# Optimization experiments

Measured on AMD Instinct MI355X. Metric: run time of the kernel, lower is better.

## Reference

```python
import jax, jax.numpy as jnp
import numpy as np

B, L, D = 2, 2048, 2048
NUM_HEADS, NUM_KV_HEADS, HEAD_DIM = 8, 4, 256
GROUPS = NUM_HEADS // NUM_KV_HEADS
ROPE_BASE, ROPE_SCALE, ROPE_PROP = 10000.0, 1.0, 1.0
WINDOW = 1024
SOFT_CAP = 50.0
K_MASK = -2.3819763e+38
EPS = 1e-6


def rms_norm(x, scale):
    # RMSNorm(head_dim, with_scale=True, scale_plus_one=False), fp32 internals
    xf = x.astype(jnp.float32)
    var = jnp.mean(jnp.square(xf), axis=-1, keepdims=True)
    return (xf * jax.lax.rsqrt(var + EPS) * scale).astype(x.dtype)


def apply_rope(x, positions):
    # x: [B, L, N, H]; Gemma-style half-split rotation over rope_proportion of H
    H = x.shape[-1]
    rope_dim = int(H * ROPE_PROP)
    half = rope_dim // 2
    freq = ROPE_BASE ** (2.0 * jnp.arange(half, dtype=jnp.float32) / rope_dim)
    t = positions.astype(jnp.float32)[:, :, None] / freq[None, None, :]  # [B,L,half]
    t = t / ROPE_SCALE
    sin = jnp.sin(t)[:, :, None, :]  # [B,L,1,half]
    cos = jnp.cos(t)[:, :, None, :]
    x1 = x[..., :half]
    x2 = x[..., half:rope_dim]
    rotated = jnp.concatenate([x1 * cos - x2 * sin, x2 * cos + x1 * sin], axis=-1)
    if rope_dim < H:
        rotated = jnp.concatenate([rotated, x[..., rope_dim:]], axis=-1)
    return rotated.astype(x.dtype)


def setup_inputs() -> dict:
    key = jax.random.key(0)
    ks = jax.random.split(key, 8)
    x = jax.random.normal(ks[0], (B, L, D), dtype=jnp.float32)
    positions = jnp.broadcast_to(jnp.arange(L, dtype=jnp.int32)[None, :], (B, L))
    attn_mask = jnp.broadcast_to(jnp.tril(jnp.ones((L, L), dtype=bool))[None], (B, L, L))
    s = 0.02
    wq = jax.random.normal(ks[1], (D, NUM_HEADS * HEAD_DIM), dtype=jnp.float32) * s
    wk = jax.random.normal(ks[2], (D, NUM_KV_HEADS * HEAD_DIM), dtype=jnp.float32) * s
    wv = jax.random.normal(ks[3], (D, NUM_KV_HEADS * HEAD_DIM), dtype=jnp.float32) * s
    wo = jax.random.normal(ks[4], (NUM_HEADS * HEAD_DIM, D), dtype=jnp.float32) * s
    q_scale = 1.0 + 0.02 * jax.random.normal(ks[5], (HEAD_DIM,), dtype=jnp.float32)
    k_scale = 1.0 + 0.02 * jax.random.normal(ks[6], (HEAD_DIM,), dtype=jnp.float32)
    return {"x": x, "positions": positions, "attn_mask": attn_mask,
            "wq": wq, "wk": wk, "wv": wv, "wo": wo,
            "q_scale": q_scale, "k_scale": k_scale}


def reference(x, positions, attn_mask, wq, wk, wv, wo, q_scale, k_scale):
    q = (x @ wq).reshape(B, L, NUM_HEADS, HEAD_DIM)
    k = (x @ wk).reshape(B, L, NUM_KV_HEADS, HEAD_DIM)
    v = (x @ wv).reshape(B, L, NUM_KV_HEADS, HEAD_DIM)
    q = rms_norm(q, q_scale)
    k = rms_norm(k, k_scale)
    q = apply_rope(q, positions)
    k = apply_rope(k, positions)
    # query_pre_attn_scalar == 1.0 in source (no-op)
    qg = q.reshape(B, L, NUM_KV_HEADS, GROUPS, HEAD_DIM)
    logits = jnp.einsum('blkgh,bskh->blkgs', qg, k).reshape(B, L, NUM_HEADS, L)
    logits = jnp.tanh(logits / SOFT_CAP) * SOFT_CAP
    # sliding-window mask (LOCAL_SLIDING, no cache -> cache_positions = positions)
    cp = positions[:, None, :]
    pp = positions[:, :, None]
    slide = (cp > pp - WINDOW) & (cp < pp + WINDOW)
    mask = attn_mask & slide  # [B, L, S]
    padded = jnp.where(mask[:, :, None, :], logits, K_MASK)
    probs = jax.nn.softmax(padded, axis=-1).astype(k.dtype)
    pg = probs.reshape(B, L, NUM_KV_HEADS, GROUPS, L)
    out = jnp.einsum('blkgs,bskh->blkgh', pg, v).reshape(B, L, NUM_HEADS * HEAD_DIM)
    return out @ wo
```

## Files before the change

kernel.cpp:

```cpp
#include <hip/hip_runtime.h>
#include <stdint.h>

typedef unsigned short u16;
typedef __bf16 bf16x8 __attribute__((ext_vector_type(8)));
typedef float f32x4 __attribute__((ext_vector_type(4)));

#define SEQ 2048
#define NH 8
#define NKVH 4
#define HD 256
#define WIN 1024
#define NBATCH 2

__device__ __forceinline__ u16 f2bf(float f) {
    union { float f; unsigned u; } v; v.f = f;
    unsigned r = v.u + 0x7FFFu + ((v.u >> 16) & 1u);
    return (u16)(r >> 16);
}
__device__ __forceinline__ float bf2f(u16 h) {
    union { unsigned u; float f; } v; v.u = ((unsigned)h) << 16;
    return v.f;
}
__device__ __forceinline__ bf16x8 ld8(const u16* p) {
    return *reinterpret_cast<const bf16x8*>(p);
}
__device__ __forceinline__ void split2(float f, u16& h, u16& l) {
    h = f2bf(f);
    l = f2bf(f - bf2f(h));
}
__device__ __forceinline__ void gld16(const u16* gp, u16* lp) {
    __builtin_amdgcn_global_load_lds(
        (__attribute__((address_space(1))) unsigned int*)gp,
        (__attribute__((address_space(3))) unsigned int*)lp, 16, 0, 0);
}
#define MFMA16(a, b, c) __builtin_amdgcn_mfma_f32_16x16x32_bf16((a), (b), (c), 0, 0, 0)

__global__ void k_cvt_x(const float* __restrict__ in, u16* __restrict__ hi,
                        u16* __restrict__ lo, int n) {
    int i = (blockIdx.x * blockDim.x + threadIdx.x) * 4;
    if (i >= n) return;
    float4 v = *reinterpret_cast<const float4*>(in + i);
    ushort4 oh, ol;
    split2(v.x, oh.x, ol.x); split2(v.y, oh.y, ol.y);
    split2(v.z, oh.z, ol.z); split2(v.w, oh.w, ol.w);
    *reinterpret_cast<ushort4*>(hi + i) = oh;
    *reinterpret_cast<ushort4*>(lo + i) = ol;
}

__global__ void k_wt(const float* __restrict__ src, u16* __restrict__ dh,
                     u16* __restrict__ dl, int ncols) {
    __shared__ float tile[64][65];
    int c0 = blockIdx.x * 64;
    int k0 = blockIdx.y * 64;
    int tx = threadIdx.x & 63, ty = threadIdx.x >> 6;
    #pragma unroll
    for (int r = 0; r < 16; ++r) {
        int k = k0 + ty * 16 + r;
        tile[ty * 16 + r][tx] = src[(size_t)k * ncols + c0 + tx];
    }
    __syncthreads();
    #pragma unroll
    for (int r = 0; r < 16; ++r) {
        int c = c0 + ty * 16 + r;
        float f = tile[tx][ty * 16 + r];
        u16 h, l; split2(f, h, l);
        dh[(size_t)c * 2048 + k0 + tx] = h;
        dl[(size_t)c * 2048 + k0 + tx] = l;
    }
}

__global__ __launch_bounds__(256, 4) void k_gemm(
        const u16* __restrict__ A0, const u16* __restrict__ B0,
        const u16* __restrict__ A1, const u16* __restrict__ B1,
        const u16* __restrict__ A2, const u16* __restrict__ B2,
        float* __restrict__ C, int M, int N, int K, int nseg, int vcol0) {
    __shared__ __align__(16) u16 sA[128 * 64];
    __shared__ __align__(16) u16 sB[128 * 64];
    const int tm = blockIdx.x * 128;
    const int tn = blockIdx.y * 128;
    const int tid = threadIdx.x;
    const int lane = tid & 63;
    const int wave = tid >> 6;
    const int wr = (wave >> 1) * 64;
    const int wc = (wave & 1) * 64;
    const int l16 = lane & 15;
    const int g = lane >> 4;
    const int srow = tid >> 3;
    const int schunk = tid & 7;
    const int nseg_eff = (tn >= vcol0) ? 1 : nseg;
    f32x4 acc[4][4] = {};

    for (int seg = 0; seg < nseg_eff; ++seg) {
        const u16* A = seg == 0 ? A0 : (seg == 1 ? A1 : A2);
        const u16* B = seg == 0 ? B0 : (seg == 1 ? B1 : B2);
        for (int k0 = 0; k0 < K; k0 += 64) {
            __syncthreads();
            #pragma unroll
            for (int i = 0; i < 4; ++i) {
                int row = i * 32 + srow;
                int cs = ((schunk ^ (row & 7)) << 3);
                gld16(A + (size_t)(tm + row) * K + k0 + cs, &sA[i * 2048 + tid * 8]);
                gld16(B + (size_t)(tn + row) * K + k0 + cs, &sB[i * 2048 + tid * 8]);
            }
            __syncthreads();
            #pragma unroll
            for (int kk = 0; kk < 2; ++kk) {
                const int j = kk * 4 + g;
                bf16x8 af[4], bfv[4];
                #pragma unroll
                for (int m = 0; m < 4; ++m) {
                    int r = wr + m * 16 + l16;
                    af[m] = ld8(&sA[r * 64 + ((j ^ (r & 7)) << 3)]);
                }
                #pragma unroll
                for (int n = 0; n < 4; ++n) {
                    int r = wc + n * 16 + l16;
                    bfv[n] = ld8(&sB[r * 64 + ((j ^ (r & 7)) << 3)]);
                }
                #pragma unroll
                for (int m = 0; m < 4; ++m)
                    #pragma unroll
                    for (int n = 0; n < 4; ++n)
                        acc[m][n] = MFMA16(af[m], bfv[n], acc[m][n]);
            }
        }
    }
    int rbase = tm + wr + g * 4;
    int cbase = tn + wc + l16;
    #pragma unroll
    for (int m = 0; m < 4; ++m)
        #pragma unroll
        for (int n = 0; n < 4; ++n)
            #pragma unroll
            for (int r = 0; r < 4; ++r)
                C[(size_t)(rbase + m * 16 + r) * N + cbase + n * 16] = acc[m][n][r];
}

__global__ __launch_bounds__(512, 2) void k_gemm256(
        const u16* __restrict__ A0, const u16* __restrict__ B0,
        const u16* __restrict__ A1, const u16* __restrict__ B1,
        const u16* __restrict__ A2, const u16* __restrict__ B2,
        float* __restrict__ C, int N, int K, int nseg, int vcol0) {
    __shared__ __align__(16) u16 sA[2][256 * 64];
    __shared__ __align__(16) u16 sB[2][256 * 64];
    const int tm = blockIdx.x * 256;
    const int tn = blockIdx.y * 256;
    const int tid = threadIdx.x;
    const int lane = tid & 63;
    const int wave = tid >> 6;
    const int wr = (wave >> 2) * 128;
    const int wc = (wave & 3) * 64;
    const int l16 = lane & 15;
    const int g = lane >> 4;
    const int nsteps = ((tn >= vcol0) ? 1 : nseg) * (K >> 6);
    const int spk = K >> 6;
    f32x4 acc[8][4] = {};

    {
        const u16* A = A0; const u16* B = B0;
        #pragma unroll
        for (int i = 0; i < 4; ++i) {
            int s = i * 512 + tid;
            int row = s >> 3, ch = s & 7;
            int cs = (ch ^ (row & 7)) << 3;
            gld16(A + (size_t)(tm + row) * K + cs, &sA[0][s * 8]);
            gld16(B + (size_t)(tn + row) * K + cs, &sB[0][s * 8]);
        }
    }
    asm volatile("s_waitcnt vmcnt(0)" ::: "memory");
    __builtin_amdgcn_s_barrier();

    int p = 0;
    for (int t = 0; t < nsteps; ++t) {
        if (t + 1 < nsteps) {
            int t1 = t + 1;
            int seg = t1 / spk;
            int k0 = (t1 - seg * spk) * 64;
            const u16* A = seg == 0 ? A0 : (seg == 1 ? A1 : A2);
            const u16* B = seg == 0 ? B0 : (seg == 1 ? B1 : B2);
            #pragma unroll
            for (int i = 0; i < 4; ++i) {
                int s = i * 512 + tid;
                int row = s >> 3, ch = s & 7;
                int cs = (ch ^ (row & 7)) << 3;
                gld16(A + (size_t)(tm + row) * K + k0 + cs, &sA[p ^ 1][s * 8]);
                gld16(B + (size_t)(tn + row) * K + k0 + cs, &sB[p ^ 1][s * 8]);
            }
        }
        __builtin_amdgcn_s_setprio(1);
        bf16x8 bfv[4][2];
        #pragma unroll
        for (int n = 0; n < 4; ++n)
            #pragma unroll
            for (int kk = 0; kk < 2; ++kk) {
                int r = wc + n * 16 + l16;
                int j = kk * 4 + g;
                bfv[n][kk] = ld8(&sB[p][r * 64 + ((j ^ (r & 7)) << 3)]);
            }
        #pragma unroll
        for (int m = 0; m < 8; ++m) {
            int r = wr + m * 16 + l16;
            bf16x8 af0 = ld8(&sA[p][r * 64 + (((0 * 4 + g) ^ (r & 7)) << 3)]);
            bf16x8 af1 = ld8(&sA[p][r * 64 + (((1 * 4 + g) ^ (r & 7)) << 3)]);
            #pragma unroll
            for (int n = 0; n < 4; ++n) {
                acc[m][n] = MFMA16(af0, bfv[n][0], acc[m][n]);
                acc[m][n] = MFMA16(af1, bfv[n][1], acc[m][n]);
            }
        }
        __builtin_amdgcn_s_setprio(0);
        asm volatile("s_waitcnt vmcnt(0) lgkmcnt(0)" ::: "memory");
        __builtin_amdgcn_sched_barrier(0);
        __builtin_amdgcn_s_barrier();
        p ^= 1;
    }

    int rbase = tm + wr + g * 4;
    int cbase = tn + wc + l16;
    #pragma unroll
    for (int m = 0; m < 8; ++m)
        #pragma unroll
        for (int n = 0; n < 4; ++n)
            #pragma unroll
            for (int r = 0; r < 4; ++r)
                C[(size_t)(rbase + m * 16 + r) * N + cbase + n * 16] = acc[m][n][r];
}

__global__ void k_normrope(const float* __restrict__ qkv, const int* __restrict__ pos,
                           const float* __restrict__ qscale, const float* __restrict__ kscale,
                           u16* __restrict__ Qh, u16* __restrict__ Ql,
                           u16* __restrict__ Kh, u16* __restrict__ Kl) {
    int wid = blockIdx.x * 4 + (threadIdx.x >> 6);
    int lane = threadIdx.x & 63;
    const int nq = NBATCH * SEQ * NH;
    const int ntot = NBATCH * SEQ * (NH + NKVH);
    if (wid >= ntot) return;
    const float* scale;
    const float* src;
    u16 *dh, *dl;
    int bt, isq;
    if (wid < nq) {
        int h = wid % NH; bt = wid / NH; isq = 1;
        scale = qscale;
        src = qkv + (size_t)bt * 4096 + h * 256;
        int b = bt >> 11, t = bt & 2047;
        size_t off = (((size_t)b * NH + h) * SEQ + t) * 256;
        dh = Qh + off; dl = Ql + off;
    } else {
        int w2 = wid - nq;
        int h = w2 % NKVH; bt = w2 / NKVH; isq = 0;
        scale = kscale;
        src = qkv + (size_t)bt * 4096 + 2048 + h * 256;
        int b = bt >> 11, t = bt & 2047;
        size_t off = (((size_t)b * NKVH + h) * SEQ + t) * 256;
        dh = Kh + off; dl = Kl + off;
    }
    const int t7 = bt & 7;
    float e[4];
    float ssq = 0.f;
    #pragma unroll
    for (int j = 0; j < 4; ++j) { e[j] = src[lane + 64 * j]; ssq += e[j] * e[j]; }
    #pragma unroll
    for (int off = 1; off < 64; off <<= 1) ssq += __shfl_xor(ssq, off);
    float inv = rsqrtf(ssq * (1.0f / 256.0f) + 1e-6f);
    #pragma unroll
    for (int j = 0; j < 4; ++j) e[j] = e[j] * inv * scale[lane + 64 * j];
    float p = (float)pos[bt];
    float fr0 = powf(10000.0f, (2.0f * lane) * (1.0f / 256.0f));
    float fr1 = powf(10000.0f, (2.0f * (lane + 64)) * (1.0f / 256.0f));
    float s0, c0, s1, c1;
    sincosf(p / fr0, &s0, &c0);
    sincosf(p / fr1, &s1, &c1);
    float rv[4];
    rv[0] = e[0] * c0 - e[2] * s0;
    rv[1] = e[1] * c1 - e[3] * s1;
    rv[2] = e[2] * c0 + e[0] * s0;
    rv[3] = e[3] * c1 + e[1] * s1;
    #pragma unroll
    for (int j = 0; j < 4; ++j) {
        int d = lane + 64 * j;
        int dd = isq ? d : ((((d >> 3) ^ t7) << 3) | (d & 7));
        u16 h, l; split2(rv[j], h, l);
        dh[dd] = h; dl[dd] = l;
    }
}

__global__ void k_vtrans(const float* __restrict__ qkv, u16* __restrict__ VT) {
    __shared__ float tile[64][65];
    int bh = blockIdx.z;
    int d0 = blockIdx.y * 64;
    int t0 = blockIdx.x * 64;
    int b = bh >> 2, h = bh & 3;
    int tx = threadIdx.x & 63, ty = threadIdx.x >> 6;
    #pragma unroll
    for (int r = 0; r < 16; ++r) {
        int t = t0 + ty * 16 + r;
        tile[ty * 16 + r][tx] = qkv[(size_t)(b * SEQ + t) * 4096 + 3072 + h * 256 + d0 + tx];
    }
    __syncthreads();
    #pragma unroll
    for (int r = 0; r < 16; ++r) {
        int d = d0 + ty * 16 + r;
        VT[((size_t)bh * 256 + d) * SEQ + t0 + tx] = f2bf(tile[tx][ty * 16 + r]);
    }
}

__global__ __launch_bounds__(256, 2) void k_attn(const u16* __restrict__ Qh, const u16* __restrict__ Ql,
                                                 const u16* __restrict__ Kh, const u16* __restrict__ Kl,
                                                 const u16* __restrict__ VT,
                                                 u16* __restrict__ Out) {
    __shared__ __align__(16) u16 sKh[32 * 256];
    __shared__ __align__(16) u16 sKl[32 * 256];
    __shared__ __align__(16) u16 sV[256 * 32];
    __shared__ __align__(16) u16 pls[4][16][40];

    const int id = blockIdx.x;
    const int xcd = id & 7;
    const int j = id >> 3;
    const int b  = xcd >> 2;
    const int hk = xcd & 3;
    const int hq = hk * 2 + (j & 1);
    const int qt = 31 - (j >> 1);
    const int tid = threadIdx.x;
    const int lane = tid & 63;
    const int wave = tid >> 6;
    const int q0b = qt * 64;
    const int q0 = q0b + wave * 16;
    const int l16 = lane & 15;
    const int g = lane >> 4;

    bf16x8 qfh[8], qfl[8];
    {
        size_t qoff = (((size_t)b * NH + hq) * SEQ + q0 + l16) * 256 + g * 8;
        #pragma unroll
        for (int kk = 0; kk < 8; ++kk) {
            qfh[kk] = ld8(Qh + qoff + kk * 32);
            qfl[kk] = ld8(Ql + qoff + kk * 32);
        }
    }

    float ssum[4] = {0.f, 0.f, 0.f, 0.f};
    f32x4 o[16] = {};

    const u16* kgh = Kh + (((size_t)b * NKVH + hk) * SEQ) * 256;
    const u16* kgl = Kl + (((size_t)b * NKVH + hk) * SEQ) * 256;
    const u16* vg  = VT + ((size_t)(b * NKVH + hk) * 256) * SEQ;

    int s_lo = q0b - (WIN - 1); if (s_lo < 0) s_lo = 0; s_lo &= ~31;
    const int s_hi = q0b + 63;
    const int ntiles = (s_hi - s_lo) / 32 + 1;

    for (int t = 0; t < ntiles; ++t) {
        const int s0 = s_lo + t * 32;
        __syncthreads();
        {
            const u16* srch = kgh + (size_t)s0 * 256 + tid * 8;
            const u16* srcl = kgl + (size_t)s0 * 256 + tid * 8;
            #pragma unroll
            for (int i = 0; i < 4; ++i) {
                gld16(srch + i * 2048, &sKh[i * 2048 + tid * 8]);
                gld16(srcl + i * 2048, &sKl[i * 2048 + tid * 8]);
            }
            const u16* srcv = vg + (size_t)(tid >> 2) * SEQ + s0 + (tid & 3) * 8;
            #pragma unroll
            for (int i = 0; i < 4; ++i)
                gld16(srcv + (size_t)i * 64 * SEQ, &sV[i * 2048 + tid * 8]);
        }
        __syncthreads();

        if (s0 <= q0 + 15 && s0 + 31 >= q0 - (WIN - 1)) {
            f32x4 c[2] = {};
            __builtin_amdgcn_s_setprio(1);
            #pragma unroll
            for (int kk = 0; kk < 8; ++kk) {
                #pragma unroll
                for (int cc = 0; cc < 2; ++cc) {
                    int row = cc * 16 + l16;
                    int slot = ((kk * 4 + g) ^ (row & 7)) << 3;
                    bf16x8 kh = ld8(&sKh[row * 256 + slot]);
                    bf16x8 kl = ld8(&sKl[row * 256 + slot]);
                    c[cc] = MFMA16(qfh[kk], kh, c[cc]);
                    c[cc] = MFMA16(qfl[kk], kh, c[cc]);
                    c[cc] = MFMA16(qfh[kk], kl, c[cc]);
                }
            }
            __builtin_amdgcn_s_setprio(0);

            const bool full = (s0 + 31 <= q0) && (s0 >= q0 + 15 - (WIN - 1));
            #pragma unroll
            for (int r = 0; r < 4; ++r) {
                int qp = q0 + g * 4 + r;
                int row = g * 4 + r;
                #pragma unroll
                for (int cc = 0; cc < 2; ++cc) {
                    float ev = __expf(c[cc][r] * 0.04f);
                    float v = 50.f - 100.f * __builtin_amdgcn_rcpf(ev + 1.f);
                    if (!full) {
                        int sp = s0 + cc * 16 + l16;
                        bool valid = (sp <= qp) && (sp > qp - WIN);
                        v = valid ? v : -1e30f;
                    }
                    float p = __expf(v - 20.f);
                    u16 pb = f2bf(p);
                    pls[wave][row][cc * 16 + l16] = pb;
                    ssum[r] += bf2f(pb);
                }
            }
            bf16x8 pa = ld8(&pls[wave][l16][g * 8]);
            __builtin_amdgcn_s_setprio(1);
            #pragma unroll
            for (int jb = 0; jb < 16; ++jb)
                o[jb] = MFMA16(pa, ld8(&sV[(jb * 16 + l16) * 32 + g * 8]), o[jb]);
            __builtin_amdgcn_s_setprio(0);
        }
    }

    #pragma unroll
    for (int off = 1; off < 16; off <<= 1)
        #pragma unroll
        for (int r = 0; r < 4; ++r) ssum[r] += __shfl_xor(ssum[r], off);
    #pragma unroll
    for (int r = 0; r < 4; ++r) {
        float inv = 1.0f / ssum[r];
        int trow = q0 + g * 4 + r;
        size_t base = ((size_t)(b * SEQ + trow) * NH + hq) * 256 + l16;
        #pragma unroll
        for (int jb = 0; jb < 16; ++jb)
            Out[base + jb * 16] = f2bf(o[jb][r] * inv);
    }
}

extern "C" void kernel_launch(void* const* d_in, const int* in_sizes, int n_in,
                              void* d_out, int out_size, void* d_ws, size_t ws_size,
                              hipStream_t stream) {
    (void)in_sizes; (void)n_in; (void)out_size; (void)ws_size;
    const float* x  = (const float*)d_in[0];
    const int* pos  = (const int*)d_in[1];
    const float* wq = (const float*)d_in[3];
    const float* wk = (const float*)d_in[4];
    const float* wv = (const float*)d_in[5];
    const float* wo = (const float*)d_in[6];
    const float* qs = (const float*)d_in[7];
    const float* ks = (const float*)d_in[8];

    const size_t MX = (size_t)4096 * 2048;
    const size_t MW = (size_t)2048 * 2048;

    u16* xh  = (u16*)d_ws;
    u16* xl  = xh + MX;
    u16* wth = xl + MX;
    u16* wtl = wth + MX;
    u16* woth = wtl + MX;
    u16* wotl = woth + MW;
    float* qkv = (float*)(wotl + MW);

    u16* qbh = xh;
    u16* qbl = qbh + MX;
    u16* kbh = qbl + MX;
    u16* kbl = kbh + MX / 2;
    u16* vt  = kbl + MX / 2;
    u16* ao  = (u16*)qkv;

    k_cvt_x<<<8192, 256, 0, stream>>>(x, xh, xl, 4096 * 2048);
    k_wt<<<dim3(32, 32), 256, 0, stream>>>(wq, wth, wtl, 2048);
    k_wt<<<dim3(16, 32), 256, 0, stream>>>(wk, wth + MW, wtl + MW, 1024);
    k_wt<<<dim3(16, 32), 256, 0, stream>>>(wv, wth + MW + MW / 2, wtl + MW + MW / 2, 1024);
    k_wt<<<dim3(32, 32), 256, 0, stream>>>(wo, woth, wotl, 2048);
    k_gemm256<<<dim3(16, 16), 512, 0, stream>>>(xh, wth, xl, wth, xh, wtl, qkv,
                                                4096, 2048, 3, 3072);
    k_normrope<<<12288, 256, 0, stream>>>(qkv, pos, qs, ks, qbh, qbl, kbh, kbl);
    k_vtrans<<<dim3(32, 4, 8), 256, 0, stream>>>(qkv, vt);
    k_attn<<<512, 256, 0, stream>>>(qbh, qbl, kbh, kbl, vt, ao);
    k_gemm<<<dim3(32, 16), 256, 0, stream>>>(ao, woth, ao, woth, ao, wotl, (float*)d_out,
                                             4096, 2048, 2048, 1, 2048);
}
```

Baseline: 381.9 us.

## Prefetch GEMM tiles two steps ahead with partial vmcnt waits

Restructures the double-buffered GEMM main loop so that loads for step t+2 are issued into the buffer just consumed, after a barrier. The wait then covers only the older batch of loads (vmcnt(8)) instead of draining every outstanding load. This keeps one tile's global loads in flight across the compute of the next step and hides more memory latency. It adds an extra barrier per iteration, and the vmcnt(8) count must stay consistent with the 8 loads each stage issues.

```diff
diff --git a/kernel.cpp b/kernel.cpp
--- a/kernel.cpp
+++ b/kernel.cpp
@@ -156,37 +156,31 @@
     const int spk = K >> 6;
     f32x4 acc[8][4] = {};
 
-    {
-        const u16* A = A0; const u16* B = B0;
+    const int srow = tid >> 3;
+    const int sch = tid & 7;
+
+    auto stage = [&](int s, int buf) {
+        int seg = s / spk;
+        int k0 = (s - seg * spk) * 64;
+        const u16* A = seg == 0 ? A0 : (seg == 1 ? A1 : A2);
+        const u16* B = seg == 0 ? B0 : (seg == 1 ? B1 : B2);
         #pragma unroll
         for (int i = 0; i < 4; ++i) {
-            int s = i * 512 + tid;
-            int row = s >> 3, ch = s & 7;
-            int cs = (ch ^ (row & 7)) << 3;
-            gld16(A + (size_t)(tm + row) * K + cs, &sA[0][s * 8]);
-            gld16(B + (size_t)(tn + row) * K + cs, &sB[0][s * 8]);
-        }
-    }
-    asm volatile("s_waitcnt vmcnt(0)" ::: "memory");
+            int row = i * 64 + srow;
+            int cs = (sch ^ (row & 7)) << 3;
+            gld16(A + (size_t)(tm + row) * K + k0 + cs, &sA[buf][(i * 512 + tid) * 8]);
+            gld16(B + (size_t)(tn + row) * K + k0 + cs, &sB[buf][(i * 512 + tid) * 8]);
+        }
+    };
+
+    stage(0, 0);
+    if (nsteps > 1) stage(1, 1);
+    asm volatile("s_waitcnt vmcnt(8)" ::: "memory");
+    if (nsteps == 1) asm volatile("s_waitcnt vmcnt(0)" ::: "memory");
     __builtin_amdgcn_s_barrier();
 
     int p = 0;
     for (int t = 0; t < nsteps; ++t) {
-        if (t + 1 < nsteps) {
-            int t1 = t + 1;
-            int seg = t1 / spk;
-            int k0 = (t1 - seg * spk) * 64;
-            const u16* A = seg == 0 ? A0 : (seg == 1 ? A1 : A2);
-            const u16* B = seg == 0 ? B0 : (seg == 1 ? B1 : B2);
-            #pragma unroll
-            for (int i = 0; i < 4; ++i) {
-                int s = i * 512 + tid;
-                int row = s >> 3, ch = s & 7;
-                int cs = (ch ^ (row & 7)) << 3;
-                gld16(A + (size_t)(tm + row) * K + k0 + cs, &sA[p ^ 1][s * 8]);
-                gld16(B + (size_t)(tn + row) * K + k0 + cs, &sB[p ^ 1][s * 8]);
-            }
-        }
         __builtin_amdgcn_s_setprio(1);
         bf16x8 bfv[4][2];
         #pragma unroll
@@ -200,8 +194,8 @@
         #pragma unroll
         for (int m = 0; m < 8; ++m) {
             int r = wr + m * 16 + l16;
-            bf16x8 af0 = ld8(&sA[p][r * 64 + (((0 * 4 + g) ^ (r & 7)) << 3)]);
-            bf16x8 af1 = ld8(&sA[p][r * 64 + (((1 * 4 + g) ^ (r & 7)) << 3)]);
+            bf16x8 af0 = ld8(&sA[p][r * 64 + ((g ^ (r & 7)) << 3)]);
+            bf16x8 af1 = ld8(&sA[p][r * 64 + (((4 + g) ^ (r & 7)) << 3)]);
             #pragma unroll
             for (int n = 0; n < 4; ++n) {
                 acc[m][n] = MFMA16(af0, bfv[n][0], acc[m][n]);
@@ -209,7 +203,14 @@
             }
         }
         __builtin_amdgcn_s_setprio(0);
-        asm volatile("s_waitcnt vmcnt(0) lgkmcnt(0)" ::: "memory");
+        __builtin_amdgcn_s_barrier();
+
+        if (t + 2 < nsteps) {
+            stage(t + 2, p);
+            asm volatile("s_waitcnt vmcnt(8)" ::: "memory");
+        } else {
+            asm volatile("s_waitcnt vmcnt(0)" ::: "memory");
+        }
         __builtin_amdgcn_sched_barrier(0);
         __builtin_amdgcn_s_barrier();
         p ^= 1;
```

Result: slower. 487.0 us (+27.5%).
